# Performance work log

Measured on AMD Instinct MI355X. Metric: run time of the kernel, lower is better.

## Reference

```python
import jax, jax.numpy as jnp
import numpy as np

N1, N2, DIM = 4096, 65536, 1024
TOPK = 4
ALPHA = 0.0


def setup_inputs() -> dict:
    key = jax.random.key(0)
    k1, k2 = jax.random.split(key)
    query_seq = jax.random.normal(k1, (N1, DIM), dtype=jnp.float32)
    synth_set = jax.random.normal(k2, (N2, DIM), dtype=jnp.float32)
    return {"query_seq": query_seq, "synth_set": synth_set}


def reference(query_seq, synth_set):
    # fast_cosine_dist: the torch code computes dot(a,b) via norm algebra
    # (-cdist^2 + |a|^2 + |b|^2)/2 == a.b ; we compute the dot product directly.
    q_norm = jnp.linalg.norm(query_seq, axis=-1)          # (N1,)
    s_norm = jnp.linalg.norm(synth_set, axis=-1)          # (N2,)
    dotprod = jnp.einsum('nd,md->nm', query_seq, synth_set)  # (N1, N2)
    dists = 1.0 - dotprod / (q_norm[:, None] * s_norm[None, :])
    # topk smallest distances (largest=False)
    _, idx = jax.lax.top_k(-dists, TOPK)                  # (N1, TOPK) int32
    knn_mean = synth_set[idx].mean(axis=1)                # (N1, DIM)
    out_feats = (1.0 - ALPHA) * knn_mean + ALPHA * query_seq
    # torch.repeat_interleave(out_feats, 2, 0) -> (2*N1, DIM)
    out_feats = jnp.repeat(out_feats, 2, axis=0)
    return out_feats
```

## Files before the change

### kernel.cpp

```cpp
#include <hip/hip_runtime.h>
#include <math.h>
#include <stdint.h>

#define N1 4096
#define N2 65536
#define DIM 1024
#define KNN 4
#define CSPLIT 32
#define BM 128
#define BN 128
#define COLS_PER_SPLIT (N2 / CSPLIT)
#define TILES_PER_SPLIT (COLS_PER_SPLIT / BN)
#define NCAND 32
#define SCSTR 68

typedef __attribute__((ext_vector_type(8))) int int32x8;
typedef __attribute__((ext_vector_type(4))) int int32x4;
typedef __attribute__((ext_vector_type(4))) float f32x4;

#define GLDS16(g, l)                                                          \
    __builtin_amdgcn_global_load_lds(                                         \
        (const __attribute__((address_space(1))) void*)(g),                   \
        (__attribute__((address_space(3))) void*)(l), 16, 0, 0)

__device__ __forceinline__ unsigned int f2fp8(float x) {
    const unsigned int u = __float_as_uint(x);
    const unsigned int s = (u >> 24) & 0x80u;
    const float ax = fminf(__uint_as_float(u & 0x7fffffffu), 448.f);
    int e = (int)(__float_as_uint(ax) >> 23) - 127;
    e = e < -6 ? -6 : e;
    const float q = rintf(ldexpf(ax, 3 - e));
    return s | (unsigned int)((e + 6) * 8 + (int)q);
}

__global__ void convert_fp8_kernel(const float* __restrict__ src,
                                   uint8_t* __restrict__ dst,
                                   float* __restrict__ invn) {
    const int t = threadIdx.x;
    const int row = blockIdx.x * 32 + (t >> 3);
    const int u = t & 7;
    const int sw = row & 7;
    const float* srow = src + ((size_t)row << 10);
    uint8_t* drow = dst + ((size_t)row << 10);
    float ss = 0.f;
#pragma unroll
    for (int k = 0; k < 8; ++k) {
        const float* p = srow + ((k * 8 + (u ^ sw)) << 4);
        unsigned int w[4];
#pragma unroll
        for (int g = 0; g < 4; ++g) {
            const float4 v = *(const float4*)(p + g * 4);
            ss += v.x * v.x + v.y * v.y + v.z * v.z + v.w * v.w;
            w[g] = f2fp8(v.x) | (f2fp8(v.y) << 8) | (f2fp8(v.z) << 16) |
                   (f2fp8(v.w) << 24);
        }
        *(uint4*)(drow + ((k * 8 + u) << 4)) = make_uint4(w[0], w[1], w[2], w[3]);
    }
#pragma unroll
    for (int off = 1; off < 8; off <<= 1) ss += __shfl_xor(ss, off, 64);
    if (invn != nullptr && u == 0) invn[row] = 1.0f / sqrtf(ss);
}

__global__ __launch_bounds__(256, 2) void gemm_topk_fp8(
    const uint8_t* __restrict__ qbf, const uint8_t* __restrict__ sbf,
    const float* __restrict__ invn, float* __restrict__ pScore,
    int* __restrict__ pIdx) {
    __shared__ __align__(16) char smem[65536];
    __shared__ float invLds[BN];
    float* const Sc = (float*)smem;

    const int tid = threadIdx.x;
    const int l = tid & 63;
    const int w = tid >> 6;
    const int waveM = w >> 1;
    const int waveN = w & 1;
    const int rowBase = blockIdx.y * BM;
    const int colSplit = blockIdx.x;
    const int colStart = colSplit * COLS_PER_SPLIT;

    const uint8_t* aSrc =
        qbf + ((size_t)(rowBase + w * 8 + (l >> 3)) << 10) + (l & 7) * 16;
    const uint8_t* bSrc0 =
        sbf + ((size_t)(colStart + w * 8 + (l >> 3)) << 10) + (l & 7) * 16;

    const int am = l & 15;
    const int q4 = l >> 4;
    const int u0 = (2 * q4) ^ (am & 7);
    const int u1 = u0 ^ 1;
    const int aBase = (waveM * 64 + am) * 128;
    const int bBase = (waveN * 64 + am) * 128;

    const unsigned int one_scales = 0x7f7f7f7fu;

    const int scanRow = tid >> 1;
    const int scanSub = tid & 1;
    float tv0 = -1e30f, tv1 = -1e30f, tv2 = -1e30f, tv3 = -1e30f;
    int ti0 = colStart, ti1 = colStart, ti2 = colStart, ti3 = colStart;
    float thr = -1e30f;

    for (int tile = 0; tile < TILES_PER_SPLIT; ++tile) {
        const int colBase = colStart + tile * BN;
        const uint8_t* bSrc = bSrc0 + ((size_t)tile << 17);
        __syncthreads();
        if (tid < BN) invLds[tid] = invn[colBase + tid];

        auto stage_st = [&](int st) {
            char* const dst = smem + (st & 1) * 32768 + w * 1024;
            const int kB = st << 7;
#pragma unroll
            for (int i = 0; i < 4; ++i) {
                GLDS16(aSrc + (size_t)i * 32768 + kB, dst + i * 4096);
                GLDS16(bSrc + (size_t)i * 32768 + kB, dst + 16384 + i * 4096);
            }
        };
        stage_st(0);
        stage_st(1);

        f32x4 acc[4][4];
#pragma unroll
        for (int i = 0; i < 4; ++i)
#pragma unroll
            for (int j = 0; j < 4; ++j) acc[i][j] = (f32x4)0.f;

#pragma unroll
        for (int st = 0; st < 8; ++st) {
            if (st < 7) asm volatile("s_waitcnt vmcnt(8)" ::: "memory");
            else        asm volatile("s_waitcnt vmcnt(0)" ::: "memory");
            __builtin_amdgcn_s_barrier();
            __builtin_amdgcn_sched_barrier(0);
            const char* const curA = smem + (st & 1) * 32768;
            const char* const curB = curA + 16384;
            int32x8 af[4], bf[4];
#pragma unroll
            for (int i = 0; i < 4; ++i) {
                const int32x4 lo = *(const int32x4*)(curA + aBase + i * 2048 + u0 * 16);
                const int32x4 hi = *(const int32x4*)(curA + aBase + i * 2048 + u1 * 16);
                af[i] = __builtin_shufflevector(lo, hi, 0, 1, 2, 3, 4, 5, 6, 7);
            }
#pragma unroll
            for (int j = 0; j < 4; ++j) {
                const int32x4 lo = *(const int32x4*)(curB + bBase + j * 2048 + u0 * 16);
                const int32x4 hi = *(const int32x4*)(curB + bBase + j * 2048 + u1 * 16);
                bf[j] = __builtin_shufflevector(lo, hi, 0, 1, 2, 3, 4, 5, 6, 7);
            }
            asm volatile("s_waitcnt lgkmcnt(0)" ::: "memory");
            __builtin_amdgcn_sched_barrier(0);
            __builtin_amdgcn_s_barrier();
            if (st < 6) stage_st(st + 2);
            __builtin_amdgcn_s_setprio(1);
#pragma unroll
            for (int i = 0; i < 4; ++i)
#pragma unroll
                for (int j = 0; j < 4; ++j)
                    acc[i][j] = __builtin_amdgcn_mfma_scale_f32_16x16x128_f8f6f4(
                        af[i], bf[j], acc[i][j], 0, 0,
                        0, one_scales, 0, one_scales);
            __builtin_amdgcn_s_setprio(0);
        }

#pragma unroll
        for (int h = 0; h < 2; ++h) {
            if (waveN == h) {
#pragma unroll
                for (int i = 0; i < 4; ++i)
#pragma unroll
                    for (int j = 0; j < 4; ++j) {
                        const float iv = invLds[h * 64 + j * 16 + am];
                        const int scCol = j * 16 + am;
#pragma unroll
                        for (int r = 0; r < 4; ++r) {
                            const int scRow = waveM * 64 + i * 16 + q4 * 4 + r;
                            Sc[scRow * SCSTR + scCol] = acc[i][j][r] * iv;
                        }
                    }
            }
            __syncthreads();
            const int sBase = scanRow * SCSTR + scanSub * 32;
#pragma unroll
            for (int c4 = 0; c4 < 8; ++c4) {
                const f32x4 v = *(const f32x4*)(Sc + sBase + c4 * 4);
                const float m4 = fmaxf(fmaxf(v[0], v[1]), fmaxf(v[2], v[3]));
                if (m4 > thr) {
#pragma unroll
                    for (int e = 0; e < 4; ++e) {
                        const float val = v[e];
                        if (val > thr) {
                            float mn = tv0; int mi = 0;
                            if (tv1 < mn) { mn = tv1; mi = 1; }
                            if (tv2 < mn) { mn = tv2; mi = 2; }
                            if (tv3 < mn) { mn = tv3; mi = 3; }
                            const int idx = colBase + h * 64 + scanSub * 32 + c4 * 4 + e;
                            if (mi == 0)      { tv0 = val; ti0 = idx; }
                            else if (mi == 1) { tv1 = val; ti1 = idx; }
                            else if (mi == 2) { tv2 = val; ti2 = idx; }
                            else              { tv3 = val; ti3 = idx; }
                            thr = fminf(fminf(tv0, tv1), fminf(tv2, tv3));
                        }
                    }
                }
            }
            if (h == 0) __syncthreads();
        }
    }

    const int prow = rowBase + scanRow;
    const size_t pbase = (((size_t)prow * CSPLIT + colSplit) * 2 + scanSub) * 4;
    pScore[pbase + 0] = tv0; pIdx[pbase + 0] = ti0;
    pScore[pbase + 1] = tv1; pIdx[pbase + 1] = ti1;
    pScore[pbase + 2] = tv2; pIdx[pbase + 2] = ti2;
    pScore[pbase + 3] = tv3; pIdx[pbase + 3] = ti3;
}

__global__ __launch_bounds__(256) void merge_rescore_gather_kernel(
    const float* __restrict__ query, const float* __restrict__ synth,
    const float* __restrict__ invn, const float* __restrict__ pScore,
    const int* __restrict__ pIdx, float* __restrict__ out) {
    const int row = blockIdx.x;
    const int t = threadIdx.x;
    const int l = t & 63;
    const int w = t >> 6;
    __shared__ float sS[256];
    __shared__ int sI[256];
    __shared__ int candIdx[NCAND];
    __shared__ float candScore[NCAND];
    __shared__ int topIdx[KNN];

    sS[t] = pScore[(size_t)row * 256 + t];
    sI[t] = pIdx[(size_t)row * 256 + t];
    __syncthreads();
    const float mv = sS[t];
    int cnt = 0;
    for (int j = 0; j < 256; ++j) {
        const float vj = sS[j];
        if (vj > mv || (vj == mv && j < t)) ++cnt;
    }
    if (cnt < NCAND) candIdx[cnt] = sI[t];
    __syncthreads();

    const float* qrow = query + ((size_t)row << 10);
#pragma unroll
    for (int u = 0; u < NCAND / 4; ++u) {
        const int cand = w * (NCAND / 4) + u;
        const int sidx = candIdx[cand];
        const float* srow = synth + ((size_t)sidx << 10);
        float ss = 0.f;
#pragma unroll
        for (int i = 0; i < 4; ++i) {
            const float4 a = *(const float4*)(qrow + l * 4 + i * 256);
            const float4 b = *(const float4*)(srow + l * 4 + i * 256);
            ss += a.x * b.x + a.y * b.y + a.z * b.z + a.w * b.w;
        }
#pragma unroll
        for (int off = 32; off > 0; off >>= 1) ss += __shfl_xor(ss, off, 64);
        if (l == 0) candScore[cand] = ss * invn[sidx];
    }
    __syncthreads();
    if (t == 0) {
        float bv0 = -1e30f, bv1 = -1e30f, bv2 = -1e30f, bv3 = -1e30f;
        int bi0 = 0, bi1 = 0, bi2 = 0, bi3 = 0;
        for (int c = 0; c < NCAND; ++c) {
            const float v = candScore[c];
            float mn = bv0; int mi = 0;
            if (bv1 < mn) { mn = bv1; mi = 1; }
            if (bv2 < mn) { mn = bv2; mi = 2; }
            if (bv3 < mn) { mn = bv3; mi = 3; }
            if (v > mn) {
                const int idx = candIdx[c];
                if (mi == 0)      { bv0 = v; bi0 = idx; }
                else if (mi == 1) { bv1 = v; bi1 = idx; }
                else if (mi == 2) { bv2 = v; bi2 = idx; }
                else              { bv3 = v; bi3 = idx; }
            }
        }
        topIdx[0] = bi0; topIdx[1] = bi1; topIdx[2] = bi2; topIdx[3] = bi3;
    }
    __syncthreads();
    const int d = t * 4;
    float4 s = make_float4(0.f, 0.f, 0.f, 0.f);
#pragma unroll
    for (int m = 0; m < KNN; ++m) {
        const float4 x = *(const float4*)(synth + ((size_t)topIdx[m] << 10) + d);
        s.x += x.x; s.y += x.y; s.z += x.z; s.w += x.w;
    }
    s.x *= 0.25f; s.y *= 0.25f; s.z *= 0.25f; s.w *= 0.25f;
    *(float4*)(out + ((size_t)(2 * row) << 10) + d) = s;
    *(float4*)(out + ((size_t)(2 * row + 1) << 10) + d) = s;
}

extern "C" void kernel_launch(void* const* d_in, const int* in_sizes, int n_in,
                              void* d_out, int out_size, void* d_ws, size_t ws_size,
                              hipStream_t stream) {
    const float* query = (const float*)d_in[0];
    const float* synth = (const float*)d_in[1];
    float* out = (float*)d_out;

    char* ws = (char*)d_ws;
    const size_t S8 = (size_t)N2 * DIM;
    const size_t Q8 = (size_t)N1 * DIM;
    const size_t INVN = (size_t)N2 * 4;
    const size_t PART = (size_t)N1 * 256 * 4;
    uint8_t* sbf = (uint8_t*)ws;
    uint8_t* qbf = (uint8_t*)(ws + S8);
    float* invn = (float*)(ws + S8 + Q8);
    float* pScore = (float*)(ws + S8 + Q8 + INVN);
    int* pIdx = (int*)(ws + S8 + Q8 + INVN + PART);

    convert_fp8_kernel<<<N2 / 32, 256, 0, stream>>>(synth, sbf, invn);
    convert_fp8_kernel<<<N1 / 32, 256, 0, stream>>>(query, qbf, nullptr);
    dim3 g1(CSPLIT, N1 / BM);
    gemm_topk_fp8<<<g1, 256, 0, stream>>>(qbf, sbf, invn, pScore, pIdx);
    merge_rescore_gather_kernel<<<N1, 256, 0, stream>>>(query, synth, invn,
                                                        pScore, pIdx, out);
}
```

Measured before the change: 1.024 ms.

## Overlap top-k scan of previous tile with MFMA of current tile; prenormalize synth fp8

```diff
diff --git a/kernel.cpp b/kernel.cpp
--- a/kernel.cpp
+++ b/kernel.cpp
@@ -12,7 +12,7 @@
 #define COLS_PER_SPLIT (N2 / CSPLIT)
 #define TILES_PER_SPLIT (COLS_PER_SPLIT / BN)
 #define NCAND 32
-#define SCSTR 68
+#define SCW 20
 
 typedef __attribute__((ext_vector_type(8))) int int32x8;
 typedef __attribute__((ext_vector_type(4))) int int32x4;
@@ -42,32 +42,43 @@
     const int sw = row & 7;
     const float* srow = src + ((size_t)row << 10);
     uint8_t* drow = dst + ((size_t)row << 10);
-    float ss = 0.f;
+    float scale = 1.0f;
+    if (invn != nullptr) {
+        float ss = 0.f;
+#pragma unroll
+        for (int k = 0; k < 8; ++k) {
+            const float* p = srow + ((k * 8 + (u ^ sw)) << 4);
+#pragma unroll
+            for (int g = 0; g < 4; ++g) {
+                const float4 v = *(const float4*)(p + g * 4);
+                ss += v.x * v.x + v.y * v.y + v.z * v.z + v.w * v.w;
+            }
+        }
+#pragma unroll
+        for (int off = 1; off < 8; off <<= 1) ss += __shfl_xor(ss, off, 64);
+        const float inv = 1.0f / sqrtf(ss);
+        scale = 16.0f * inv;
+        if (u == 0) invn[row] = inv;
+    }
 #pragma unroll
     for (int k = 0; k < 8; ++k) {
         const float* p = srow + ((k * 8 + (u ^ sw)) << 4);
-        unsigned int w[4];
+        unsigned int wv[4];
 #pragma unroll
         for (int g = 0; g < 4; ++g) {
             const float4 v = *(const float4*)(p + g * 4);
-            ss += v.x * v.x + v.y * v.y + v.z * v.z + v.w * v.w;
-            w[g] = f2fp8(v.x) | (f2fp8(v.y) << 8) | (f2fp8(v.z) << 16) |
-                   (f2fp8(v.w) << 24);
-        }
-        *(uint4*)(drow + ((k * 8 + u) << 4)) = make_uint4(w[0], w[1], w[2], w[3]);
-    }
-#pragma unroll
-    for (int off = 1; off < 8; off <<= 1) ss += __shfl_xor(ss, off, 64);
-    if (invn != nullptr && u == 0) invn[row] = 1.0f / sqrtf(ss);
+            wv[g] = f2fp8(v.x * scale) | (f2fp8(v.y * scale) << 8) |
+                    (f2fp8(v.z * scale) << 16) | (f2fp8(v.w * scale) << 24);
+        }
+        *(uint4*)(drow + ((k * 8 + u) << 4)) = make_uint4(wv[0], wv[1], wv[2], wv[3]);
+    }
 }
 
 __global__ __launch_bounds__(256, 2) void gemm_topk_fp8(
     const uint8_t* __restrict__ qbf, const uint8_t* __restrict__ sbf,
-    const float* __restrict__ invn, float* __restrict__ pScore,
-    int* __restrict__ pIdx) {
+    float* __restrict__ pScore, int* __restrict__ pIdx) {
     __shared__ __align__(16) char smem[65536];
-    __shared__ float invLds[BN];
-    float* const Sc = (float*)smem;
+    __shared__ __align__(16) float Sc[BM * SCW];
 
     const int tid = threadIdx.x;
     const int l = tid & 63;
@@ -93,39 +104,59 @@
     const unsigned int one_scales = 0x7f7f7f7fu;
 
     const int scanRow = tid >> 1;
-    const int scanSub = tid & 1;
+    const int sub = tid & 1;
     float tv0 = -1e30f, tv1 = -1e30f, tv2 = -1e30f, tv3 = -1e30f;
     int ti0 = colStart, ti1 = colStart, ti2 = colStart, ti3 = colStart;
     float thr = -1e30f;
 
+    auto insert4 = [&](float val, int idx) {
+        float mn = tv0; int mi = 0;
+        if (tv1 < mn) { mn = tv1; mi = 1; }
+        if (tv2 < mn) { mn = tv2; mi = 2; }
+        if (tv3 < mn) { mn = tv3; mi = 3; }
+        if (mi == 0)      { tv0 = val; ti0 = idx; }
+        else if (mi == 1) { tv1 = val; ti1 = idx; }
+        else if (mi == 2) { tv2 = val; ti2 = idx; }
+        else              { tv3 = val; ti3 = idx; }
+        thr = fminf(fminf(tv0, tv1), fminf(tv2, tv3));
+    };
+    auto scanCmp = [&](const f32x4 v, int ibase) {
+        const float m4 = fmaxf(fmaxf(v[0], v[1]), fmaxf(v[2], v[3]));
+        if (m4 > thr) {
+#pragma unroll
+            for (int e = 0; e < 4; ++e)
+                if (v[e] > thr) insert4(v[e], ibase + e);
+        }
+    };
+
+    auto stageTo = [&](const uint8_t* bSrcT, int st) {
+        char* const dst = smem + (st & 1) * 32768 + w * 1024;
+        const int kB = (st & 7) << 7;
+#pragma unroll
+        for (int i = 0; i < 4; ++i) {
+            GLDS16(aSrc + (size_t)i * 32768 + kB, dst + i * 4096);
+            GLDS16(bSrcT + (size_t)i * 32768 + kB, dst + 16384 + i * 4096);
+        }
+    };
+
+    f32x4 acc[4][4], eacc[4][4];
+#pragma unroll
+    for (int i = 0; i < 4; ++i)
+#pragma unroll
+        for (int j = 0; j < 4; ++j) acc[i][j] = (f32x4)0.f;
+    int cbA = 0, cbB = 0;
+
+    stageTo(bSrc0, 0);
+    stageTo(bSrc0, 1);
+
     for (int tile = 0; tile < TILES_PER_SPLIT; ++tile) {
-        const int colBase = colStart + tile * BN;
         const uint8_t* bSrc = bSrc0 + ((size_t)tile << 17);
-        __syncthreads();
-        if (tid < BN) invLds[tid] = invn[colBase + tid];
-
-        auto stage_st = [&](int st) {
-            char* const dst = smem + (st & 1) * 32768 + w * 1024;
-            const int kB = st << 7;
-#pragma unroll
-            for (int i = 0; i < 4; ++i) {
-                GLDS16(aSrc + (size_t)i * 32768 + kB, dst + i * 4096);
-                GLDS16(bSrc + (size_t)i * 32768 + kB, dst + 16384 + i * 4096);
-            }
-        };
-        stage_st(0);
-        stage_st(1);
-
-        f32x4 acc[4][4];
-#pragma unroll
-        for (int i = 0; i < 4; ++i)
-#pragma unroll
-            for (int j = 0; j < 4; ++j) acc[i][j] = (f32x4)0.f;
-
+        const bool wrEn = (tile >= 1);
 #pragma unroll
         for (int st = 0; st < 8; ++st) {
             if (st < 7) asm volatile("s_waitcnt vmcnt(8)" ::: "memory");
             else        asm volatile("s_waitcnt vmcnt(0)" ::: "memory");
+            asm volatile("s_waitcnt lgkmcnt(0)" ::: "memory");
             __builtin_amdgcn_s_barrier();
             __builtin_amdgcn_sched_barrier(0);
             const char* const curA = smem + (st & 1) * 32768;
@@ -143,10 +174,45 @@
                 const int32x4 hi = *(const int32x4*)(curB + bBase + j * 2048 + u1 * 16);
                 bf[j] = __builtin_shufflevector(lo, hi, 0, 1, 2, 3, 4, 5, 6, 7);
             }
+            const int p = (st + 7) & 7;
+            const bool scEn = (st == 0) ? (tile >= 2) : (tile >= 1);
+            f32x4 sv0 = (f32x4)0.f, sv1 = (f32x4)0.f;
+            int sb = 0;
+            if (scEn) {
+                const float* srow = Sc + scanRow * SCW + sub * 8;
+                sv0 = *(const f32x4*)srow;
+                sv1 = *(const f32x4*)(srow + 4);
+                sb = ((st == 0) ? cbB : cbA) + ((p & 1) << 6) + ((p >> 1) << 4) + sub * 8;
+            }
             asm volatile("s_waitcnt lgkmcnt(0)" ::: "memory");
             __builtin_amdgcn_sched_barrier(0);
             __builtin_amdgcn_s_barrier();
-            if (st < 6) stage_st(st + 2);
+            if (st < 6) {
+                stageTo(bSrc, st + 2);
+            } else if (st == 7) {
+                if (tile + 1 < TILES_PER_SPLIT) {
+                    const uint8_t* bn = bSrc0 + ((size_t)(tile + 1) << 17);
+                    stageTo(bn, 0);
+                    stageTo(bn, 1);
+                }
+                if (wrEn && waveN == 1) {
+#pragma unroll
+                    for (int i = 0; i < 4; ++i)
+#pragma unroll
+                        for (int r = 0; r < 4; ++r)
+                            Sc[(waveM * 64 + i * 16 + q4 * 4 + r) * SCW + am] =
+                                eacc[i][3][r];
+                }
+            }
+            if (st < 7 && wrEn && waveN == (st & 1)) {
+                const int j = st >> 1;
+#pragma unroll
+                for (int i = 0; i < 4; ++i)
+#pragma unroll
+                    for (int r = 0; r < 4; ++r)
+                        Sc[(waveM * 64 + i * 16 + q4 * 4 + r) * SCW + am] =
+                            eacc[i][j][r];
+            }
             __builtin_amdgcn_s_setprio(1);
 #pragma unroll
             for (int i = 0; i < 4; ++i)
@@ -156,55 +222,53 @@
                         af[i], bf[j], acc[i][j], 0, 0,
                         0, one_scales, 0, one_scales);
             __builtin_amdgcn_s_setprio(0);
-        }
-
-#pragma unroll
-        for (int h = 0; h < 2; ++h) {
-            if (waveN == h) {
+            if (scEn) { scanCmp(sv0, sb); scanCmp(sv1, sb + 4); }
+            if (st == 7) {
 #pragma unroll
                 for (int i = 0; i < 4; ++i)
 #pragma unroll
                     for (int j = 0; j < 4; ++j) {
-                        const float iv = invLds[h * 64 + j * 16 + am];
-                        const int scCol = j * 16 + am;
-#pragma unroll
-                        for (int r = 0; r < 4; ++r) {
-                            const int scRow = waveM * 64 + i * 16 + q4 * 4 + r;
-                            Sc[scRow * SCSTR + scCol] = acc[i][j][r] * iv;
-                        }
+                        eacc[i][j] = acc[i][j];
+                        acc[i][j] = (f32x4)0.f;
                     }
-            }
-            __syncthreads();
-            const int sBase = scanRow * SCSTR + scanSub * 32;
-#pragma unroll
-            for (int c4 = 0; c4 < 8; ++c4) {
-                const f32x4 v = *(const f32x4*)(Sc + sBase + c4 * 4);
-                const float m4 = fmaxf(fmaxf(v[0], v[1]), fmaxf(v[2], v[3]));
-                if (m4 > thr) {
-#pragma unroll
-                    for (int e = 0; e < 4; ++e) {
-                        const float val = v[e];
-                        if (val > thr) {
-                            float mn = tv0; int mi = 0;
-                            if (tv1 < mn) { mn = tv1; mi = 1; }
-                            if (tv2 < mn) { mn = tv2; mi = 2; }
-                            if (tv3 < mn) { mn = tv3; mi = 3; }
-                            const int idx = colBase + h * 64 + scanSub * 32 + c4 * 4 + e;
-                            if (mi == 0)      { tv0 = val; ti0 = idx; }
-                            else if (mi == 1) { tv1 = val; ti1 = idx; }
-                            else if (mi == 2) { tv2 = val; ti2 = idx; }
-                            else              { tv3 = val; ti3 = idx; }
-                            thr = fminf(fminf(tv0, tv1), fminf(tv2, tv3));
-                        }
-                    }
-                }
-            }
-            if (h == 0) __syncthreads();
-        }
+                cbB = cbA;
+                cbA = colStart + tile * BN;
+            }
+        }
+    }
+
+    __syncthreads();
+    {
+        const float* srow = Sc + scanRow * SCW + sub * 8;
+        const f32x4 a = *(const f32x4*)srow;
+        const f32x4 b = *(const f32x4*)(srow + 4);
+        const int sb = cbB + 64 + 48 + sub * 8;
+        scanCmp(a, sb);
+        scanCmp(b, sb + 4);
+    }
+    __syncthreads();
+#pragma unroll
+    for (int pp = 0; pp < 8; ++pp) {
+        if (waveN == (pp & 1)) {
+            const int j = pp >> 1;
+#pragma unroll
+            for (int i = 0; i < 4; ++i)
+#pragma unroll
+                for (int r = 0; r < 4; ++r)
+                    Sc[(waveM * 64 + i * 16 + q4 * 4 + r) * SCW + am] = eacc[i][j][r];
+        }
+        __syncthreads();
+        const float* srow = Sc + scanRow * SCW + sub * 8;
+        const f32x4 a = *(const f32x4*)srow;
+        const f32x4 b = *(const f32x4*)(srow + 4);
+        const int sb = cbA + ((pp & 1) << 6) + ((pp >> 1) << 4) + sub * 8;
+        scanCmp(a, sb);
+        scanCmp(b, sb + 4);
+        __syncthreads();
     }
 
     const int prow = rowBase + scanRow;
-    const size_t pbase = (((size_t)prow * CSPLIT + colSplit) * 2 + scanSub) * 4;
+    const size_t pbase = (((size_t)prow * CSPLIT + colSplit) * 2 + sub) * 4;
     pScore[pbase + 0] = tv0; pIdx[pbase + 0] = ti0;
     pScore[pbase + 1] = tv1; pIdx[pbase + 1] = ti1;
     pScore[pbase + 2] = tv2; pIdx[pbase + 2] = ti2;
@@ -308,7 +372,7 @@
     convert_fp8_kernel<<<N2 / 32, 256, 0, stream>>>(synth, sbf, invn);
     convert_fp8_kernel<<<N1 / 32, 256, 0, stream>>>(query, qbf, nullptr);
     dim3 g1(CSPLIT, N1 / BM);
-    gemm_topk_fp8<<<g1, 256, 0, stream>>>(qbf, sbf, invn, pScore, pIdx);
+    gemm_topk_fp8<<<g1, 256, 0, stream>>>(qbf, sbf, pScore, pIdx);
     merge_rescore_gather_kernel<<<N1, 256, 0, stream>>>(query, synth, invn,
                                                         pScore, pIdx, out);
 }
```

Measured after the change: 2.103 ms. 2.05x slower.

## Pre-normalize synth rows in fp8, load query fragments directly to registers

Applied to the files above, without the earlier changes.

```diff
diff --git a/kernel.cpp b/kernel.cpp
--- a/kernel.cpp
+++ b/kernel.cpp
@@ -39,35 +39,46 @@
     const int t = threadIdx.x;
     const int row = blockIdx.x * 32 + (t >> 3);
     const int u = t & 7;
-    const int sw = row & 7;
+    const int sw = (invn != nullptr) ? (row & 7) : 0;
     const float* srow = src + ((size_t)row << 10);
     uint8_t* drow = dst + ((size_t)row << 10);
-    float ss = 0.f;
+    float scale = 1.0f;
+    if (invn != nullptr) {
+        float ss = 0.f;
+#pragma unroll
+        for (int k = 0; k < 8; ++k) {
+            const float* p = srow + ((k * 8 + (u ^ sw)) << 4);
+#pragma unroll
+            for (int g = 0; g < 4; ++g) {
+                const float4 v = *(const float4*)(p + g * 4);
+                ss += v.x * v.x + v.y * v.y + v.z * v.z + v.w * v.w;
+            }
+        }
+#pragma unroll
+        for (int off = 1; off < 8; off <<= 1) ss += __shfl_xor(ss, off, 64);
+        const float inv = 1.0f / sqrtf(ss);
+        scale = 16.0f * inv;
+        if (u == 0) invn[row] = inv;
+    }
 #pragma unroll
     for (int k = 0; k < 8; ++k) {
         const float* p = srow + ((k * 8 + (u ^ sw)) << 4);
-        unsigned int w[4];
+        unsigned int wv[4];
 #pragma unroll
         for (int g = 0; g < 4; ++g) {
             const float4 v = *(const float4*)(p + g * 4);
-            ss += v.x * v.x + v.y * v.y + v.z * v.z + v.w * v.w;
-            w[g] = f2fp8(v.x) | (f2fp8(v.y) << 8) | (f2fp8(v.z) << 16) |
-                   (f2fp8(v.w) << 24);
-        }
-        *(uint4*)(drow + ((k * 8 + u) << 4)) = make_uint4(w[0], w[1], w[2], w[3]);
-    }
-#pragma unroll
-    for (int off = 1; off < 8; off <<= 1) ss += __shfl_xor(ss, off, 64);
-    if (invn != nullptr && u == 0) invn[row] = 1.0f / sqrtf(ss);
+            wv[g] = f2fp8(v.x * scale) | (f2fp8(v.y * scale) << 8) |
+                    (f2fp8(v.z * scale) << 16) | (f2fp8(v.w * scale) << 24);
+        }
+        *(uint4*)(drow + ((k * 8 + u) << 4)) = make_uint4(wv[0], wv[1], wv[2], wv[3]);
+    }
 }
 
 __global__ __launch_bounds__(256, 2) void gemm_topk_fp8(
     const uint8_t* __restrict__ qbf, const uint8_t* __restrict__ sbf,
-    const float* __restrict__ invn, float* __restrict__ pScore,
-    int* __restrict__ pIdx) {
-    __shared__ __align__(16) char smem[65536];
-    __shared__ float invLds[BN];
-    float* const Sc = (float*)smem;
+    float* __restrict__ pScore, int* __restrict__ pIdx) {
+    __shared__ __align__(16) char Bs[32768];
+    __shared__ __align__(16) float Sc[BM * SCSTR];
 
     const int tid = threadIdx.x;
     const int l = tid & 63;
@@ -78,65 +89,88 @@
     const int colSplit = blockIdx.x;
     const int colStart = colSplit * COLS_PER_SPLIT;
 
-    const uint8_t* aSrc =
-        qbf + ((size_t)(rowBase + w * 8 + (l >> 3)) << 10) + (l & 7) * 16;
     const uint8_t* bSrc0 =
         sbf + ((size_t)(colStart + w * 8 + (l >> 3)) << 10) + (l & 7) * 16;
 
     const int am = l & 15;
     const int q4 = l >> 4;
+    const uint8_t* aPtr =
+        qbf + ((size_t)(rowBase + waveM * 64 + am) << 10) + q4 * 32;
     const int u0 = (2 * q4) ^ (am & 7);
     const int u1 = u0 ^ 1;
-    const int aBase = (waveM * 64 + am) * 128;
     const int bBase = (waveN * 64 + am) * 128;
 
     const unsigned int one_scales = 0x7f7f7f7fu;
 
     const int scanRow = tid >> 1;
-    const int scanSub = tid & 1;
+    const int sub = tid & 1;
     float tv0 = -1e30f, tv1 = -1e30f, tv2 = -1e30f, tv3 = -1e30f;
     int ti0 = colStart, ti1 = colStart, ti2 = colStart, ti3 = colStart;
     float thr = -1e30f;
 
+    auto insert4 = [&](float val, int idx) {
+        float mn = tv0; int mi = 0;
+        if (tv1 < mn) { mn = tv1; mi = 1; }
+        if (tv2 < mn) { mn = tv2; mi = 2; }
+        if (tv3 < mn) { mn = tv3; mi = 3; }
+        if (mi == 0)      { tv0 = val; ti0 = idx; }
+        else if (mi == 1) { tv1 = val; ti1 = idx; }
+        else if (mi == 2) { tv2 = val; ti2 = idx; }
+        else              { tv3 = val; ti3 = idx; }
+        thr = fminf(fminf(tv0, tv1), fminf(tv2, tv3));
+    };
+    auto scanCmp = [&](const f32x4 v, int ibase) {
+        const float m4 = fmaxf(fmaxf(v[0], v[1]), fmaxf(v[2], v[3]));
+        if (m4 > thr) {
+#pragma unroll
+            for (int e = 0; e < 4; ++e)
+                if (v[e] > thr) insert4(v[e], ibase + e);
+        }
+    };
+
+    auto stageB = [&](const uint8_t* bT, int s) {
+        char* const dst = Bs + (s & 1) * 16384 + w * 1024;
+        const int kB = s << 7;
+#pragma unroll
+        for (int i = 0; i < 4; ++i)
+            GLDS16(bT + (size_t)i * 32768 + kB, dst + i * 4096);
+    };
+
+    int32x8 af[2][4];
+    f32x4 acc[4][4];
+#pragma unroll
+    for (int i = 0; i < 4; ++i)
+#pragma unroll
+        for (int j = 0; j < 4; ++j) acc[i][j] = (f32x4)0.f;
+
+    stageB(bSrc0, 0);
+    __builtin_amdgcn_sched_barrier(0);
+#pragma unroll
+    for (int i = 0; i < 4; ++i)
+        af[0][i] = *(const int32x8*)(aPtr + i * 16384);
+    __builtin_amdgcn_sched_barrier(0);
+    stageB(bSrc0, 1);
+    __builtin_amdgcn_sched_barrier(0);
+
     for (int tile = 0; tile < TILES_PER_SPLIT; ++tile) {
+        const uint8_t* bSrc = bSrc0 + ((size_t)tile << 17);
+        const uint8_t* bSrcN =
+            bSrc0 + ((size_t)(tile + 1 < TILES_PER_SPLIT ? tile + 1 : tile) << 17);
         const int colBase = colStart + tile * BN;
-        const uint8_t* bSrc = bSrc0 + ((size_t)tile << 17);
-        __syncthreads();
-        if (tid < BN) invLds[tid] = invn[colBase + tid];
-
-        auto stage_st = [&](int st) {
-            char* const dst = smem + (st & 1) * 32768 + w * 1024;
-            const int kB = st << 7;
-#pragma unroll
-            for (int i = 0; i < 4; ++i) {
-                GLDS16(aSrc + (size_t)i * 32768 + kB, dst + i * 4096);
-                GLDS16(bSrc + (size_t)i * 32768 + kB, dst + 16384 + i * 4096);
-            }
-        };
-        stage_st(0);
-        stage_st(1);
-
-        f32x4 acc[4][4];
-#pragma unroll
-        for (int i = 0; i < 4; ++i)
-#pragma unroll
-            for (int j = 0; j < 4; ++j) acc[i][j] = (f32x4)0.f;
-
 #pragma unroll
         for (int st = 0; st < 8; ++st) {
-            if (st < 7) asm volatile("s_waitcnt vmcnt(8)" ::: "memory");
-            else        asm volatile("s_waitcnt vmcnt(0)" ::: "memory");
+            asm volatile("s_waitcnt vmcnt(4)" ::: "memory");
             __builtin_amdgcn_s_barrier();
             __builtin_amdgcn_sched_barrier(0);
-            const char* const curA = smem + (st & 1) * 32768;
-            const char* const curB = curA + 16384;
-            int32x8 af[4], bf[4];
-#pragma unroll
-            for (int i = 0; i < 4; ++i) {
-                const int32x4 lo = *(const int32x4*)(curA + aBase + i * 2048 + u0 * 16);
-                const int32x4 hi = *(const int32x4*)(curA + aBase + i * 2048 + u1 * 16);
-                af[i] = __builtin_shufflevector(lo, hi, 0, 1, 2, 3, 4, 5, 6, 7);
-            }
+            {
+                const int kA = ((st + 1) & 7) << 7;
+#pragma unroll
+                for (int i = 0; i < 4; ++i)
+                    af[(st + 1) & 1][i] =
+                        *(const int32x8*)(aPtr + i * 16384 + kA);
+            }
+            const char* const curB = Bs + (st & 1) * 16384;
+            int32x8 bf[4];
 #pragma unroll
             for (int j = 0; j < 4; ++j) {
                 const int32x4 lo = *(const int32x4*)(curB + bBase + j * 2048 + u0 * 16);
@@ -146,14 +180,15 @@
             asm volatile("s_waitcnt lgkmcnt(0)" ::: "memory");
             __builtin_amdgcn_sched_barrier(0);
             __builtin_amdgcn_s_barrier();
-            if (st < 6) stage_st(st + 2);
+            if (st < 6) stageB(bSrc, st + 2);
+            else        stageB(bSrcN, st - 6);
             __builtin_amdgcn_s_setprio(1);
 #pragma unroll
             for (int i = 0; i < 4; ++i)
 #pragma unroll
                 for (int j = 0; j < 4; ++j)
                     acc[i][j] = __builtin_amdgcn_mfma_scale_f32_16x16x128_f8f6f4(
-                        af[i], bf[j], acc[i][j], 0, 0,
+                        af[st & 1][i], bf[j], acc[i][j], 0, 0,
                         0, one_scales, 0, one_scales);
             __builtin_amdgcn_s_setprio(0);
         }
@@ -165,46 +200,36 @@
                 for (int i = 0; i < 4; ++i)
 #pragma unroll
                     for (int j = 0; j < 4; ++j) {
-                        const float iv = invLds[h * 64 + j * 16 + am];
                         const int scCol = j * 16 + am;
 #pragma unroll
-                        for (int r = 0; r < 4; ++r) {
-                            const int scRow = waveM * 64 + i * 16 + q4 * 4 + r;
-                            Sc[scRow * SCSTR + scCol] = acc[i][j][r] * iv;
-                        }
+                        for (int r = 0; r < 4; ++r)
+                            Sc[(waveM * 64 + i * 16 + q4 * 4 + r) * SCSTR + scCol] =
+                                acc[i][j][r];
                     }
             }
-            __syncthreads();
-            const int sBase = scanRow * SCSTR + scanSub * 32;
-#pragma unroll
-            for (int c4 = 0; c4 < 8; ++c4) {
-                const f32x4 v = *(const f32x4*)(Sc + sBase + c4 * 4);
-                const float m4 = fmaxf(fmaxf(v[0], v[1]), fmaxf(v[2], v[3]));
-                if (m4 > thr) {
-#pragma unroll
-                    for (int e = 0; e < 4; ++e) {
-                        const float val = v[e];
-                        if (val > thr) {
-                            float mn = tv0; int mi = 0;
-                            if (tv1 < mn) { mn = tv1; mi = 1; }
-                            if (tv2 < mn) { mn = tv2; mi = 2; }
-                            if (tv3 < mn) { mn = tv3; mi = 3; }
-                            const int idx = colBase + h * 64 + scanSub * 32 + c4 * 4 + e;
-                            if (mi == 0)      { tv0 = val; ti0 = idx; }
-                            else if (mi == 1) { tv1 = val; ti1 = idx; }
-                            else if (mi == 2) { tv2 = val; ti2 = idx; }
-                            else              { tv3 = val; ti3 = idx; }
-                            thr = fminf(fminf(tv0, tv1), fminf(tv2, tv3));
-                        }
-                    }
+            asm volatile("s_waitcnt lgkmcnt(0)" ::: "memory");
+            __builtin_amdgcn_s_barrier();
+            {
+                const float* srow = Sc + scanRow * SCSTR + sub * 32;
+                const int base = colBase + h * 64 + sub * 32;
+#pragma unroll
+                for (int c4 = 0; c4 < 8; ++c4) {
+                    const f32x4 v = *(const f32x4*)(srow + c4 * 4);
+                    scanCmp(v, base + c4 * 4);
                 }
             }
-            if (h == 0) __syncthreads();
-        }
-    }
-
+            asm volatile("s_waitcnt lgkmcnt(0)" ::: "memory");
+            __builtin_amdgcn_s_barrier();
+        }
+#pragma unroll
+        for (int i = 0; i < 4; ++i)
+#pragma unroll
+            for (int j = 0; j < 4; ++j) acc[i][j] = (f32x4)0.f;
+    }
+
+    asm volatile("s_waitcnt vmcnt(0)" ::: "memory");
     const int prow = rowBase + scanRow;
-    const size_t pbase = (((size_t)prow * CSPLIT + colSplit) * 2 + scanSub) * 4;
+    const size_t pbase = (((size_t)prow * CSPLIT + colSplit) * 2 + sub) * 4;
     pScore[pbase + 0] = tv0; pIdx[pbase + 0] = ti0;
     pScore[pbase + 1] = tv1; pIdx[pbase + 1] = ti1;
     pScore[pbase + 2] = tv2; pIdx[pbase + 2] = ti2;
@@ -308,7 +333,7 @@
     convert_fp8_kernel<<<N2 / 32, 256, 0, stream>>>(synth, sbf, invn);
     convert_fp8_kernel<<<N1 / 32, 256, 0, stream>>>(query, qbf, nullptr);
     dim3 g1(CSPLIT, N1 / BM);
-    gemm_topk_fp8<<<g1, 256, 0, stream>>>(qbf, sbf, invn, pScore, pIdx);
+    gemm_topk_fp8<<<g1, 256, 0, stream>>>(qbf, sbf, pScore, pIdx);
     merge_rescore_gather_kernel<<<N1, 256, 0, stream>>>(query, synth, invn,
                                                         pScore, pIdx, out);
 }
```

Measured after the change: 1.773 ms. +73.2%, slower.

## Pre-normalize synth rows before FP8 quantization and drop in-GEMM norm scaling

Applied to the files above, without the earlier changes.

```diff
diff --git a/kernel.cpp b/kernel.cpp
--- a/kernel.cpp
+++ b/kernel.cpp
@@ -42,31 +42,42 @@
     const int sw = row & 7;
     const float* srow = src + ((size_t)row << 10);
     uint8_t* drow = dst + ((size_t)row << 10);
-    float ss = 0.f;
+    float scale = 1.0f;
+    if (invn != nullptr) {
+        float ss = 0.f;
+#pragma unroll
+        for (int k = 0; k < 8; ++k) {
+            const float* p = srow + ((k * 8 + (u ^ sw)) << 4);
+#pragma unroll
+            for (int g = 0; g < 4; ++g) {
+                const float4 v = *(const float4*)(p + g * 4);
+                ss += v.x * v.x + v.y * v.y + v.z * v.z + v.w * v.w;
+            }
+        }
+#pragma unroll
+        for (int off = 1; off < 8; off <<= 1) ss += __shfl_xor(ss, off, 64);
+        const float inv = 1.0f / sqrtf(ss);
+        scale = 16.0f * inv;
+        if (u == 0) invn[row] = inv;
+    }
 #pragma unroll
     for (int k = 0; k < 8; ++k) {
         const float* p = srow + ((k * 8 + (u ^ sw)) << 4);
-        unsigned int w[4];
+        unsigned int wv[4];
 #pragma unroll
         for (int g = 0; g < 4; ++g) {
             const float4 v = *(const float4*)(p + g * 4);
-            ss += v.x * v.x + v.y * v.y + v.z * v.z + v.w * v.w;
-            w[g] = f2fp8(v.x) | (f2fp8(v.y) << 8) | (f2fp8(v.z) << 16) |
-                   (f2fp8(v.w) << 24);
-        }
-        *(uint4*)(drow + ((k * 8 + u) << 4)) = make_uint4(w[0], w[1], w[2], w[3]);
-    }
-#pragma unroll
-    for (int off = 1; off < 8; off <<= 1) ss += __shfl_xor(ss, off, 64);
-    if (invn != nullptr && u == 0) invn[row] = 1.0f / sqrtf(ss);
+            wv[g] = f2fp8(v.x * scale) | (f2fp8(v.y * scale) << 8) |
+                    (f2fp8(v.z * scale) << 16) | (f2fp8(v.w * scale) << 24);
+        }
+        *(uint4*)(drow + ((k * 8 + u) << 4)) = make_uint4(wv[0], wv[1], wv[2], wv[3]);
+    }
 }
 
 __global__ __launch_bounds__(256, 2) void gemm_topk_fp8(
     const uint8_t* __restrict__ qbf, const uint8_t* __restrict__ sbf,
-    const float* __restrict__ invn, float* __restrict__ pScore,
-    int* __restrict__ pIdx) {
+    float* __restrict__ pScore, int* __restrict__ pIdx) {
     __shared__ __align__(16) char smem[65536];
-    __shared__ float invLds[BN];
     float* const Sc = (float*)smem;
 
     const int tid = threadIdx.x;
@@ -87,32 +98,51 @@
     const int q4 = l >> 4;
     const int u0 = (2 * q4) ^ (am & 7);
     const int u1 = u0 ^ 1;
-    const int aBase = (waveM * 64 + am) * 128;
-    const int bBase = (waveN * 64 + am) * 128;
+    const int aOff = (waveM * 64 + am) * 128;
+    const int bOff = (waveN * 64 + am) * 128;
 
     const unsigned int one_scales = 0x7f7f7f7fu;
 
     const int scanRow = tid >> 1;
-    const int scanSub = tid & 1;
+    const int sub = tid & 1;
     float tv0 = -1e30f, tv1 = -1e30f, tv2 = -1e30f, tv3 = -1e30f;
     int ti0 = colStart, ti1 = colStart, ti2 = colStart, ti3 = colStart;
     float thr = -1e30f;
 
+    auto insert4 = [&](float val, int idx) {
+        float mn = tv0; int mi = 0;
+        if (tv1 < mn) { mn = tv1; mi = 1; }
+        if (tv2 < mn) { mn = tv2; mi = 2; }
+        if (tv3 < mn) { mn = tv3; mi = 3; }
+        if (mi == 0)      { tv0 = val; ti0 = idx; }
+        else if (mi == 1) { tv1 = val; ti1 = idx; }
+        else if (mi == 2) { tv2 = val; ti2 = idx; }
+        else              { tv3 = val; ti3 = idx; }
+        thr = fminf(fminf(tv0, tv1), fminf(tv2, tv3));
+    };
+    auto scanCmp = [&](const f32x4 v, int ibase) {
+        const float m4 = fmaxf(fmaxf(v[0], v[1]), fmaxf(v[2], v[3]));
+        if (m4 > thr) {
+#pragma unroll
+            for (int e = 0; e < 4; ++e)
+                if (v[e] > thr) insert4(v[e], ibase + e);
+        }
+    };
+
     for (int tile = 0; tile < TILES_PER_SPLIT; ++tile) {
         const int colBase = colStart + tile * BN;
         const uint8_t* bSrc = bSrc0 + ((size_t)tile << 17);
-        __syncthreads();
-        if (tid < BN) invLds[tid] = invn[colBase + tid];
 
         auto stage_st = [&](int st) {
             char* const dst = smem + (st & 1) * 32768 + w * 1024;
-            const int kB = st << 7;
+            const int kB = st * 128;
 #pragma unroll
             for (int i = 0; i < 4; ++i) {
                 GLDS16(aSrc + (size_t)i * 32768 + kB, dst + i * 4096);
                 GLDS16(bSrc + (size_t)i * 32768 + kB, dst + 16384 + i * 4096);
             }
         };
+        __syncthreads();
         stage_st(0);
         stage_st(1);
 
@@ -133,29 +163,27 @@
             int32x8 af[4], bf[4];
 #pragma unroll
             for (int i = 0; i < 4; ++i) {
-                const int32x4 lo = *(const int32x4*)(curA + aBase + i * 2048 + u0 * 16);
-                const int32x4 hi = *(const int32x4*)(curA + aBase + i * 2048 + u1 * 16);
+                const int32x4 lo = *(const int32x4*)(curA + aOff + i * 2048 + u0 * 16);
+                const int32x4 hi = *(const int32x4*)(curA + aOff + i * 2048 + u1 * 16);
                 af[i] = __builtin_shufflevector(lo, hi, 0, 1, 2, 3, 4, 5, 6, 7);
             }
 #pragma unroll
             for (int j = 0; j < 4; ++j) {
-                const int32x4 lo = *(const int32x4*)(curB + bBase + j * 2048 + u0 * 16);
-                const int32x4 hi = *(const int32x4*)(curB + bBase + j * 2048 + u1 * 16);
+                const int32x4 lo = *(const int32x4*)(curB + bOff + j * 2048 + u0 * 16);
+                const int32x4 hi = *(const int32x4*)(curB + bOff + j * 2048 + u1 * 16);
                 bf[j] = __builtin_shufflevector(lo, hi, 0, 1, 2, 3, 4, 5, 6, 7);
             }
+#pragma unroll
+            for (int i = 0; i < 4; ++i)
+#pragma unroll
+                for (int j = 0; j < 4; ++j)
+                    acc[i][j] = __builtin_amdgcn_mfma_scale_f32_16x16x128_f8f6f4(
+                        af[i], bf[j], acc[i][j], 0, 0,
+                        0, one_scales, 0, one_scales);
             asm volatile("s_waitcnt lgkmcnt(0)" ::: "memory");
             __builtin_amdgcn_sched_barrier(0);
             __builtin_amdgcn_s_barrier();
             if (st < 6) stage_st(st + 2);
-            __builtin_amdgcn_s_setprio(1);
-#pragma unroll
-            for (int i = 0; i < 4; ++i)
-#pragma unroll
-                for (int j = 0; j < 4; ++j)
-                    acc[i][j] = __builtin_amdgcn_mfma_scale_f32_16x16x128_f8f6f4(
-                        af[i], bf[j], acc[i][j], 0, 0,
-                        0, one_scales, 0, one_scales);
-            __builtin_amdgcn_s_setprio(0);
         }
 
 #pragma unroll
@@ -165,38 +193,21 @@
                 for (int i = 0; i < 4; ++i)
 #pragma unroll
                     for (int j = 0; j < 4; ++j) {
-                        const float iv = invLds[h * 64 + j * 16 + am];
                         const int scCol = j * 16 + am;
 #pragma unroll
-                        for (int r = 0; r < 4; ++r) {
-                            const int scRow = waveM * 64 + i * 16 + q4 * 4 + r;
-                            Sc[scRow * SCSTR + scCol] = acc[i][j][r] * iv;
-                        }
+                        for (int r = 0; r < 4; ++r)
+                            Sc[(waveM * 64 + i * 16 + q4 * 4 + r) * SCSTR + scCol] =
+                                acc[i][j][r];
                     }
             }
             __syncthreads();
-            const int sBase = scanRow * SCSTR + scanSub * 32;
-#pragma unroll
-            for (int c4 = 0; c4 < 8; ++c4) {
-                const f32x4 v = *(const f32x4*)(Sc + sBase + c4 * 4);
-                const float m4 = fmaxf(fmaxf(v[0], v[1]), fmaxf(v[2], v[3]));
-                if (m4 > thr) {
-#pragma unroll
-                    for (int e = 0; e < 4; ++e) {
-                        const float val = v[e];
-                        if (val > thr) {
-                            float mn = tv0; int mi = 0;
-                            if (tv1 < mn) { mn = tv1; mi = 1; }
-                            if (tv2 < mn) { mn = tv2; mi = 2; }
-                            if (tv3 < mn) { mn = tv3; mi = 3; }
-                            const int idx = colBase + h * 64 + scanSub * 32 + c4 * 4 + e;
-                            if (mi == 0)      { tv0 = val; ti0 = idx; }
-                            else if (mi == 1) { tv1 = val; ti1 = idx; }
-                            else if (mi == 2) { tv2 = val; ti2 = idx; }
-                            else              { tv3 = val; ti3 = idx; }
-                            thr = fminf(fminf(tv0, tv1), fminf(tv2, tv3));
-                        }
-                    }
+            {
+                const float* srow = Sc + scanRow * SCSTR + sub * 32;
+                const int base = colBase + h * 64 + sub * 32;
+#pragma unroll
+                for (int c4 = 0; c4 < 8; ++c4) {
+                    const f32x4 v = *(const f32x4*)(srow + c4 * 4);
+                    scanCmp(v, base + c4 * 4);
                 }
             }
             if (h == 0) __syncthreads();
@@ -204,7 +215,7 @@
     }
 
     const int prow = rowBase + scanRow;
-    const size_t pbase = (((size_t)prow * CSPLIT + colSplit) * 2 + scanSub) * 4;
+    const size_t pbase = (((size_t)prow * CSPLIT + colSplit) * 2 + sub) * 4;
     pScore[pbase + 0] = tv0; pIdx[pbase + 0] = ti0;
     pScore[pbase + 1] = tv1; pIdx[pbase + 1] = ti1;
     pScore[pbase + 2] = tv2; pIdx[pbase + 2] = ti2;
@@ -308,7 +319,7 @@
     convert_fp8_kernel<<<N2 / 32, 256, 0, stream>>>(synth, sbf, invn);
     convert_fp8_kernel<<<N1 / 32, 256, 0, stream>>>(query, qbf, nullptr);
     dim3 g1(CSPLIT, N1 / BM);
-    gemm_topk_fp8<<<g1, 256, 0, stream>>>(qbf, sbf, invn, pScore, pIdx);
+    gemm_topk_fp8<<<g1, 256, 0, stream>>>(qbf, sbf, pScore, pIdx);
     merge_rescore_gather_kernel<<<N1, 256, 0, stream>>>(query, synth, invn,
                                                         pScore, pIdx, out);
 }
```

Result: slower. 1.394 ms (+36.2%).
